# Kernel tuning notes

Measured on AMD Instinct MI355X. Metric: run time of the kernel, lower is better.

The kernel has to match this reference:

```python
import jax, jax.numpy as jnp
import numpy as np

N = 100000
E = 1600000
D = 128  # out_dim == head_dim (num_heads = 1)


def setup_inputs() -> dict:
    key = jax.random.key(0)
    ks = jax.random.split(key, 16)
    s = 0.05
    inp = {
        "h": jax.random.normal(ks[0], (N, D), dtype=jnp.float32),
        "c": jax.random.normal(ks[1], (N, 3), dtype=jnp.float32),
        "src": jax.random.randint(ks[2], (E,), 0, N),
        "dst": jax.random.randint(ks[3], (E,), 0, N),
        # Q/K/V projections (use_bias=False)
        "Wq": jax.random.normal(ks[4], (D, D), dtype=jnp.float32) * s,
        "Wk": jax.random.normal(ks[5], (D, D), dtype=jnp.float32) * s,
        "Wv": jax.random.normal(ks[6], (D, D), dtype=jnp.float32) * s,
        # linear_p: Linear(3,3) -> ReLU -> Linear(3,D)
        "Wp1": jax.random.normal(ks[7], (3, 3), dtype=jnp.float32) * s,
        "bp1": jnp.zeros((3,), dtype=jnp.float32),
        "Wp2": jax.random.normal(ks[8], (3, D), dtype=jnp.float32) * s,
        "bp2": jnp.zeros((D,), dtype=jnp.float32),
        # edge MLP: Linear(D,D) -> ReLU -> Linear(D,1)
        "We1": jax.random.normal(ks[9], (D, D), dtype=jnp.float32) * s,
        "be1": jnp.zeros((D,), dtype=jnp.float32),
        "We2": jax.random.normal(ks[10], (D, 1), dtype=jnp.float32) * s,
        "be2": jnp.zeros((1,), dtype=jnp.float32),
        # output projection O (has bias)
        "Wo": jax.random.normal(ks[11], (D, D), dtype=jnp.float32) * s,
        "bo": jnp.zeros((D,), dtype=jnp.float32),
    }
    return inp


def reference(h, c, src, dst, Wq, Wk, Wv, Wp1, bp1, Wp2, bp2,
              We1, be1, We2, be2, Wo, bo):
    scale = np.sqrt(np.float32(D))  # sqrt(out_dim) used by scaled_exp
    n = h.shape[0]
    # node projections
    Q = h @ Wq                                   # [N, D]
    K = h @ Wk                                   # [N, D]
    V = h @ Wv                                   # [N, D]
    P = jax.nn.relu(c @ Wp1 + bp1) @ Wp2 + bp2   # [N, D] position encoding
    # per-edge point-transformer score: MLP(K[src] - Q[dst] + P[src])
    dif = K[src] - Q[dst] + P[src]               # [E, D]
    raw = jax.nn.relu(dif @ We1 + be1) @ We2 + be2  # [E, 1]
    score = jnp.exp(jnp.clip(raw / scale, -5.0, 5.0))  # [E, 1]
    # gather-multiply-scatter: weighted V+P sum and normalizer z per dst node
    msg = (V + P)[src] * score                   # [E, D]
    wV = jax.ops.segment_sum(msg, dst, num_segments=n)    # [N, D]
    z = jax.ops.segment_sum(score, dst, num_segments=n)   # [N, 1]
    head_out = wV / z                            # [N, D]
    return head_out @ Wo + bo                    # [N, D]
```

## Files before the change

### kernel.cpp

```cpp
#include <hip/hip_runtime.h>
#include <math.h>

#define DD 128
#define CAP 10240
typedef unsigned int u32;
typedef unsigned short u16;
typedef __attribute__((ext_vector_type(8))) short bf16x8;
typedef __attribute__((ext_vector_type(4))) float f32x4;
typedef __attribute__((ext_vector_type(2))) float f32x2;

__device__ __forceinline__ float4 f4zero() { return make_float4(0.f, 0.f, 0.f, 0.f); }
__device__ __forceinline__ u32 bf16rne(float f) {
    u32 u = __float_as_uint(f);
    u += 0x7FFFu + ((u >> 16) & 1u);
    return u >> 16;
}
__device__ __forceinline__ u32 pack2(float lo, float hi) {
    return bf16rne(lo) | (bf16rne(hi) << 16);
}
__device__ __forceinline__ float unlo(u32 u) { return __uint_as_float(u << 16); }
__device__ __forceinline__ float unhi(u32 u) { return __uint_as_float(u & 0xFFFF0000u); }

__global__ __launch_bounds__(256) void fused_pre(
    const float* __restrict__ Wq, const float* __restrict__ Wk,
    const float* __restrict__ Wv, const float* __restrict__ We1,
    const float* __restrict__ be1, const float* __restrict__ Wp2,
    const float* __restrict__ bp2, const float* __restrict__ Wo,
    u32* __restrict__ BF,
    const int* __restrict__ src, const int* __restrict__ dst,
    int* __restrict__ gcount, u32* __restrict__ ebuf, int E) {
    const int t = threadIdx.x;
    if (blockIdx.x < 38) {
        const int bid = blockIdx.x * 4 + (t >> 6);
        const int l = t & 63;
        const int c = l & 15;
        const int kg = l >> 4;
        float val[8];

        if (bid < 120) {
            const int ct = bid / 5, ks = bid - ct * 5;
            const int u = ct / 6, r = ct - u * 6;
            const int n = 32 * u + 16 * (r < 2 ? r : (r & 1)) + c;
#pragma unroll
            for (int j = 0; j < 8; ++j) {
                const int k = ks * 32 + kg * 8 + j;
                float v = 0.f;
                if (r < 2) {
                    if (k < 128) {
                        float a = 0.f;
                        for (int q = 0; q < 128; ++q)
                            a = fmaf(Wq[k * 128 + q], We1[q * 128 + n], a);
                        v = a;
                    }
                } else if (r < 4) {
                    if (k < 128) {
                        float a = 0.f;
                        for (int q = 0; q < 128; ++q)
                            a = fmaf(Wk[k * 128 + q], We1[q * 128 + n], a);
                        v = a;
                    } else if (k < 131) {
                        float a = 0.f;
                        for (int q = 0; q < 128; ++q)
                            a = fmaf(Wp2[(k - 128) * 128 + q], We1[q * 128 + n], a);
                        v = a;
                    } else if (k == 131) {
                        float a = be1[n];
                        for (int q = 0; q < 128; ++q)
                            a = fmaf(bp2[q], We1[q * 128 + n], a);
                        v = a;
                    }
                } else {
                    if (k < 128) v = Wv[k * 128 + n];
                    else if (k < 131) v = Wp2[(k - 128) * 128 + n];
                    else if (k == 131) v = bp2[n];
                }
                val[j] = v;
            }
        } else {
            const int b2 = bid - 120;
            const int ct = b2 >> 2, ks = b2 & 3;
            const int n = ct * 16 + c;
#pragma unroll
            for (int j = 0; j < 8; ++j) {
                const int k = ks * 32 + kg * 8 + j;
                val[j] = Wo[k * 128 + n];
            }
        }
        u32* dp = &BF[((size_t)bid * 64 + l) * 4];
        dp[0] = pack2(val[0], val[1]);
        dp[1] = pack2(val[2], val[3]);
        dp[2] = pack2(val[4], val[5]);
        dp[3] = pack2(val[6], val[7]);
    } else {
        __shared__ int hist[256];
        __shared__ int base[256];
        hist[t] = 0;
        __syncthreads();
        const int chunk = (blockIdx.x - 38) * 4096;
        int bk[16], rk[16];
        u32 pv[16];
#pragma unroll
        for (int i = 0; i < 16; ++i) {
            int idx = chunk + i * 256 + t;
            bk[i] = -1;
            if (idx < E) {
                int dd = dst[idx];
                int ss = src[idx];
                bk[i] = dd >> 9;
                pv[i] = ((u32)ss << 9) | (u32)(dd & 511);
                rk[i] = atomicAdd(&hist[bk[i]], 1);
            }
        }
        __syncthreads();
        if (hist[t]) base[t] = t * CAP + atomicAdd(&gcount[t], hist[t]);
        __syncthreads();
#pragma unroll
        for (int i = 0; i < 16; ++i) {
            if (bk[i] >= 0) ebuf[base[bk[i]] + rk[i]] = pv[i];
        }
    }
}

__global__ __launch_bounds__(256) void scanB_we2r(
    const int* __restrict__ gcount, int* __restrict__ bucket_base,
    const float* __restrict__ We2, float* __restrict__ We2r) {
    __shared__ int s[256];
    int t = threadIdx.x;
    int orig = gcount[t];
    s[t] = orig;
    __syncthreads();
    for (int off = 1; off < 256; off <<= 1) {
        int x = (t >= off) ? s[t - off] : 0;
        __syncthreads();
        s[t] += x;
        __syncthreads();
    }
    bucket_base[t] = s[t] - orig;
    if (t < 128) {
        int col = 32 * (t >> 5) + 16 * (t & 1) + ((t & 31) >> 1);
        We2r[t] = We2[col];
    }
}

__global__ __launch_bounds__(256) void fused_mid(
    const float* __restrict__ h, const float* __restrict__ c,
    const float* __restrict__ Wp1, const float* __restrict__ bp1,
    const u32* __restrict__ BF,
    u32* __restrict__ QWb, u32* __restrict__ Vb,
    unsigned char* __restrict__ Kb8, int N,
    const int* __restrict__ gcount, const int* __restrict__ bucket_base,
    const u32* __restrict__ ebuf, int* __restrict__ ssrc,
    int* __restrict__ offs, int E, int NR) {
    __shared__ u32 lds[64 * 96];
    const int t = threadIdx.x;

    if ((int)blockIdx.x < NR) {
        int* cnt = (int*)lds;
        int* cur = cnt + 512;
        int* ts = cur + 512;
        const int r = blockIdx.x;
        const int cnt_r = gcount[r];
        const int base_r = bucket_base[r];
        cnt[t] = 0;
        cnt[t + 256] = 0;
        __syncthreads();
        const u32* eb = &ebuf[(size_t)r * CAP];
        for (int i = t; i < cnt_r; i += 256) atomicAdd(&cnt[eb[i] & 511], 1);
        __syncthreads();
        int v0 = cnt[2 * t], v1 = cnt[2 * t + 1];
        int pair = v0 + v1;
        ts[t] = pair;
        __syncthreads();
        for (int off = 1; off < 256; off <<= 1) {
            int x = (t >= off) ? ts[t - off] : 0;
            __syncthreads();
            ts[t] += x;
            __syncthreads();
        }
        int ex = ts[t] - pair;
        cur[2 * t] = ex;
        cur[2 * t + 1] = ex + v0;
        offs[r * 512 + 2 * t] = base_r + ex;
        offs[r * 512 + 2 * t + 1] = base_r + ex + v0;
        if (r == NR - 1 && t == 255) offs[NR * 512] = E;
        __syncthreads();
        for (int i = t; i < cnt_r; i += 256) {
            u32 e = eb[i];
            int p = atomicAdd(&cur[e & 511], 1);
            ssrc[base_r + p] = (int)(e >> 9);
        }
    } else {
        u32* hs = lds;
        const int row0 = ((int)blockIdx.x - NR) * 64;

#pragma unroll
        for (int i = 0; i < 8; ++i) {
            int f = t + i * 256;
            int row = f >> 5;
            int cq = f & 31;
            float4 v = f4zero();
            if (row0 + row < N) v = *(const float4*)&h[(size_t)(row0 + row) * DD + cq * 4];
            int idx = row * 96 + ((cq * 2) ^ ((row & 7) << 2));
            uint2 p;
            p.x = pack2(v.x, v.y);
            p.y = pack2(v.z, v.w);
            *(uint2*)&hs[idx] = p;
        }
        if (t < 64) {
            int row = t;
            float u0 = 0.f, u1 = 0.f, u2 = 0.f;
            if (row0 + row < N) {
                const float* cr = &c[(size_t)(row0 + row) * 3];
                float c0 = cr[0], c1 = cr[1], c2 = cr[2];
                u0 = fmaxf(bp1[0] + c0 * Wp1[0] + c1 * Wp1[3] + c2 * Wp1[6], 0.f);
                u1 = fmaxf(bp1[1] + c0 * Wp1[1] + c1 * Wp1[4] + c2 * Wp1[7], 0.f);
                u2 = fmaxf(bp1[2] + c0 * Wp1[2] + c1 * Wp1[5] + c2 * Wp1[8], 0.f);
            }
            int swz = (row & 7) << 2;
            uint4 z0 = make_uint4(pack2(u0, u1), pack2(u2, 1.0f), 0u, 0u);
            uint4 zz = make_uint4(0u, 0u, 0u, 0u);
#pragma unroll
            for (int q = 0; q < 4; ++q) {
                int idx = row * 96 + 64 + ((q * 4) ^ swz);
                *(uint4*)&hs[idx] = (q == 0) ? z0 : zz;
            }
        }
        __syncthreads();

        const int w = t >> 6, l = t & 63;
        const int cc = l & 15, kg = l >> 4;

        f32x4 acc[4][6];
#pragma unroll
        for (int rt = 0; rt < 4; ++rt)
#pragma unroll
            for (int r = 0; r < 6; ++r) acc[rt][r] = (f32x4){0.f, 0.f, 0.f, 0.f};

#pragma unroll
        for (int ks = 0; ks < 5; ++ks) {
            bf16x8 a[4];
#pragma unroll
            for (int rt = 0; rt < 4; ++rt) {
                int row = rt * 16 + cc;
                int idx = row * 96 + ((ks * 16 + kg * 4) ^ ((row & 7) << 2));
                a[rt] = *(const bf16x8*)&hs[idx];
            }
#pragma unroll
            for (int r = 0; r < 6; ++r) {
                const bf16x8 b = *(const bf16x8*)&BF[(((size_t)(w * 6 + r) * 5 + ks) * 64 + l) * 4];
#pragma unroll
                for (int rt = 0; rt < 4; ++rt)
                    acc[rt][r] = __builtin_amdgcn_mfma_f32_16x16x32_bf16(a[rt], b, acc[rt][r], 0, 0, 0);
            }
        }

#pragma unroll
        for (int rt = 0; rt < 4; ++rt) {
#pragma unroll
            for (int j = 0; j < 4; ++j) {
                int row = row0 + rt * 16 + kg * 4 + j;
                if (row >= N) continue;
                QWb[(size_t)row * 64 + w * 16 + cc] = pack2(acc[rt][0][j], acc[rt][1][j]);
                Vb[(size_t)row * 64 + w * 16 + cc] = pack2(acc[rt][4][j], acc[rt][5][j]);
                u32 kp = __builtin_amdgcn_cvt_pk_fp8_f32(acc[rt][2][j], acc[rt][3][j], 0u, false);
                *(u16*)&Kb8[(size_t)row * 128 + w * 32 + cc * 2] = (u16)kp;
            }
        }
    }
}

__global__ __launch_bounds__(256) void aggregate(
    const int* __restrict__ offs, const int* __restrict__ ssrc,
    const unsigned char* __restrict__ Kb8, const u32* __restrict__ Vb,
    const u32* __restrict__ QWb, const float* __restrict__ We2r,
    const float* __restrict__ be2, u32* __restrict__ headb, int N) {
    const int node = (blockIdx.x * 256 + threadIdx.x) >> 6;
    const int lane = threadIdx.x & 63;
    if (node >= N) return;
    const int g = lane >> 4, i = lane & 15;

    const float INVS = 0.08838834764831845f;

    uint4 Qu = *(const uint4*)&QWb[(size_t)node * 64 + 4 * i];
    float q0 = unlo(Qu.x), q1 = unhi(Qu.x), q2 = unlo(Qu.y), q3 = unhi(Qu.y);
    float q4 = unlo(Qu.z), q5 = unhi(Qu.z), q6 = unlo(Qu.w), q7 = unhi(Qu.w);
    float4 wA = *(const float4*)&We2r[8 * i];
    float4 wB = *(const float4*)&We2r[8 * i + 4];
    float b2 = be2[0];

    const int beg = offs[node], end = offs[node + 1];
    float a0 = 0.f, a1 = 0.f, a2 = 0.f, a3 = 0.f;
    float a4 = 0.f, a5 = 0.f, a6 = 0.f, a7 = 0.f;
    float zacc = 0.f;

    int e = beg + g;
    int s = (e < end) ? ssrc[e] : 0;
    for (int e0 = beg; e0 < end; e0 += 4) {
        const bool act = (e0 + g) < end;
        const int scur = s;
        const int en = e0 + 4 + g;
        s = (en < end) ? ssrc[en] : 0;

        uint2 kk = *(const uint2*)&Kb8[(size_t)scur * 128 + 8 * i];
        uint4 va = *(const uint4*)&Vb[(size_t)scur * 64 + 4 * i];

        f32x2 f0 = __builtin_amdgcn_cvt_pk_f32_fp8(kk.x, false);
        f32x2 f1 = __builtin_amdgcn_cvt_pk_f32_fp8(kk.x, true);
        f32x2 f2 = __builtin_amdgcn_cvt_pk_f32_fp8(kk.y, false);
        f32x2 f3 = __builtin_amdgcn_cvt_pk_f32_fp8(kk.y, true);

        float p;
        p = fmaxf(f0[0] - q0, 0.f) * wA.x;
        p = fmaf(fmaxf(f0[1] - q1, 0.f), wA.y, p);
        p = fmaf(fmaxf(f1[0] - q2, 0.f), wA.z, p);
        p = fmaf(fmaxf(f1[1] - q3, 0.f), wA.w, p);
        p = fmaf(fmaxf(f2[0] - q4, 0.f), wB.x, p);
        p = fmaf(fmaxf(f2[1] - q5, 0.f), wB.y, p);
        p = fmaf(fmaxf(f3[0] - q6, 0.f), wB.z, p);
        p = fmaf(fmaxf(f3[1] - q7, 0.f), wB.w, p);
#pragma unroll
        for (int off = 1; off <= 8; off <<= 1) p += __shfl_xor(p, off);

        float sc = act ? __expf(fminf(fmaxf((p + b2) * INVS, -5.f), 5.f)) : 0.f;

        a0 = fmaf(unlo(va.x), sc, a0);
        a1 = fmaf(unhi(va.x), sc, a1);
        a2 = fmaf(unlo(va.y), sc, a2);
        a3 = fmaf(unhi(va.y), sc, a3);
        a4 = fmaf(unlo(va.z), sc, a4);
        a5 = fmaf(unhi(va.z), sc, a5);
        a6 = fmaf(unlo(va.w), sc, a6);
        a7 = fmaf(unhi(va.w), sc, a7);
        zacc += sc;
    }

    a0 += __shfl_xor(a0, 16); a0 += __shfl_xor(a0, 32);
    a1 += __shfl_xor(a1, 16); a1 += __shfl_xor(a1, 32);
    a2 += __shfl_xor(a2, 16); a2 += __shfl_xor(a2, 32);
    a3 += __shfl_xor(a3, 16); a3 += __shfl_xor(a3, 32);
    a4 += __shfl_xor(a4, 16); a4 += __shfl_xor(a4, 32);
    a5 += __shfl_xor(a5, 16); a5 += __shfl_xor(a5, 32);
    a6 += __shfl_xor(a6, 16); a6 += __shfl_xor(a6, 32);
    a7 += __shfl_xor(a7, 16); a7 += __shfl_xor(a7, 32);
    zacc += __shfl_xor(zacc, 16); zacc += __shfl_xor(zacc, 32);

    if (g == 0) {
        float rz = 1.0f / zacc;
        uint4 o;
        o.x = pack2(a0 * rz, a1 * rz);
        o.y = pack2(a2 * rz, a3 * rz);
        o.z = pack2(a4 * rz, a5 * rz);
        o.w = pack2(a6 * rz, a7 * rz);
        *(uint4*)&headb[(size_t)node * 64 + 4 * i] = o;
    }
}

__global__ __launch_bounds__(256) void out_mfma(
    const u32* __restrict__ headb, const u32* __restrict__ WoF,
    const float* __restrict__ bo, float* __restrict__ out, int N) {
    __shared__ u32 hs[64 * 64];

    const int row0 = blockIdx.x * 64;
    const int t = threadIdx.x;

#pragma unroll
    for (int i = 0; i < 4; ++i) {
        int f = t + i * 256;
        int row = f >> 4;
        int cq = f & 15;
        uint4 v = make_uint4(0u, 0u, 0u, 0u);
        if (row0 + row < N) v = *(const uint4*)&headb[(size_t)(row0 + row) * 64 + cq * 4];
        int m = cq >> 2;
        int cb = (cq & 3) * 4;
        int swz = (row & 7) << 2;
        uint2 A, B;
        A.x = (v.x & 0xFFFFu) | (v.y << 16);
        A.y = (v.z & 0xFFFFu) | (v.w << 16);
        B.x = (v.x >> 16) | (v.y & 0xFFFF0000u);
        B.y = (v.z >> 16) | (v.w & 0xFFFF0000u);
        int dA = 16 * m + (cb >> 1);
        *(uint2*)&hs[row * 64 + (dA ^ swz)] = A;
        *(uint2*)&hs[row * 64 + ((dA + 8) ^ swz)] = B;
    }
    __syncthreads();

    const int w = t >> 6, l = t & 63;
    const int cc = l & 15, kg = l >> 4;

    f32x4 acc[4][2];
#pragma unroll
    for (int rt = 0; rt < 4; ++rt) {
        acc[rt][0] = (f32x4){0.f, 0.f, 0.f, 0.f};
        acc[rt][1] = (f32x4){0.f, 0.f, 0.f, 0.f};
    }

#pragma unroll
    for (int ks = 0; ks < 4; ++ks) {
        bf16x8 a[4];
#pragma unroll
        for (int rt = 0; rt < 4; ++rt) {
            int row = rt * 16 + cc;
            int idx = row * 64 + ((ks * 16 + kg * 4) ^ ((row & 7) << 2));
            a[rt] = *(const bf16x8*)&hs[idx];
        }
#pragma unroll
        for (int ctl = 0; ctl < 2; ++ctl) {
            const bf16x8 b = *(const bf16x8*)&WoF[(((size_t)(2 * w + ctl) * 4 + ks) * 64 + l) * 4];
#pragma unroll
            for (int rt = 0; rt < 4; ++rt)
                acc[rt][ctl] = __builtin_amdgcn_mfma_f32_16x16x32_bf16(a[rt], b, acc[rt][ctl], 0, 0, 0);
        }
    }

#pragma unroll
    for (int ctl = 0; ctl < 2; ++ctl) {
        int col = (2 * w + ctl) * 16 + cc;
        float bias = bo[col];
#pragma unroll
        for (int rt = 0; rt < 4; ++rt) {
#pragma unroll
            for (int j = 0; j < 4; ++j) {
                int row = row0 + rt * 16 + kg * 4 + j;
                if (row >= N) continue;
                out[(size_t)row * DD + col] = acc[rt][ctl][j] + bias;
            }
        }
    }
}

extern "C" void kernel_launch(void* const* d_in, const int* in_sizes, int n_in,
                              void* d_out, int out_size, void* d_ws, size_t ws_size,
                              hipStream_t stream) {
    const float* h   = (const float*)d_in[0];
    const float* c   = (const float*)d_in[1];
    const int*   src = (const int*)d_in[2];
    const int*   dst = (const int*)d_in[3];
    const float* Wq  = (const float*)d_in[4];
    const float* Wk  = (const float*)d_in[5];
    const float* Wv  = (const float*)d_in[6];
    const float* Wp1 = (const float*)d_in[7];
    const float* bp1 = (const float*)d_in[8];
    const float* Wp2 = (const float*)d_in[9];
    const float* bp2 = (const float*)d_in[10];
    const float* We1 = (const float*)d_in[11];
    const float* be1 = (const float*)d_in[12];
    const float* We2 = (const float*)d_in[13];
    const float* be2 = (const float*)d_in[14];
    const float* Wo  = (const float*)d_in[15];
    const float* bo  = (const float*)d_in[16];

    const int N = in_sizes[0] / DD;
    const int E = in_sizes[2];
    const int NR = (N + 511) >> 9;

    u32* BF    = (u32*)d_ws;
    u32* WoF   = BF + 120 * 256;
    u32* QWb   = BF + 152 * 256;
    u32* Vb    = QWb + (size_t)N * 64;
    unsigned char* Kb8 = (unsigned char*)(Vb + (size_t)N * 64);
    u32* headb = (u32*)(Kb8 + (size_t)N * 128);
    int* offs  = (int*)(headb + (size_t)N * 64);
    int* gcount = offs + ((size_t)NR * 512 + 1);
    int* bbase  = gcount + 256;
    float* We2r = (float*)(bbase + 256);
    int* ssrc   = (int*)(We2r + 128);
    u32* ebuf   = (u32*)(ssrc + E);

    const int NB1 = (E + 4095) / 4096;

    hipMemsetAsync(gcount, 0, 256 * sizeof(int), stream);

    fused_pre<<<38 + NB1, 256, 0, stream>>>(Wq, Wk, Wv, We1, be1, Wp2, bp2, Wo,
                                            BF, src, dst, gcount, ebuf, E);

    scanB_we2r<<<1, 256, 0, stream>>>(gcount, bbase, We2, We2r);

    fused_mid<<<NR + (N + 63) / 64, 256, 0, stream>>>(
        h, c, Wp1, bp1, BF, QWb, Vb, Kb8, N,
        gcount, bbase, ebuf, ssrc, offs, E, NR);

    aggregate<<<(N * 64 + 255) / 256, 256, 0, stream>>>(offs, ssrc, Kb8, Vb,
                                                        QWb, We2r, be2, headb, N);

    out_mfma<<<(N + 63) / 64, 256, 0, stream>>>(headb, WoF, bo, (float*)d_out, N);
}
```

Baseline: 210.1 us.

## Regroup pipeline kernels and widen per-lane work in edge aggregation

Splits weight-fragment composition into its own small kernel and fuses the edge bucketing pass with the node projection GEMM. The local per-bucket sort moves into a separate kernel after the scan. The aggregate kernel now has each lane handle 16 features with 8 edges in flight per node, using exp2 with a prescaled constant. Workspace layout is reordered. This changes kernel overlap and memory-level parallelism in the gather, at the cost of an extra launch and higher register pressure.

After: 236.5 us. 1.13x slower.

```diff
diff --git a/kernel.cpp b/kernel.cpp
--- a/kernel.cpp
+++ b/kernel.cpp
@@ -21,82 +21,92 @@
 __device__ __forceinline__ float unlo(u32 u) { return __uint_as_float(u << 16); }
 __device__ __forceinline__ float unhi(u32 u) { return __uint_as_float(u & 0xFFFF0000u); }
 
-__global__ __launch_bounds__(256) void fused_pre(
+__global__ __launch_bounds__(256) void compose_frags(
     const float* __restrict__ Wq, const float* __restrict__ Wk,
     const float* __restrict__ Wv, const float* __restrict__ We1,
     const float* __restrict__ be1, const float* __restrict__ Wp2,
     const float* __restrict__ bp2, const float* __restrict__ Wo,
-    u32* __restrict__ BF,
+    u32* __restrict__ BF) {
+    const int t = threadIdx.x;
+    const int bid = blockIdx.x * 4 + (t >> 6);
+    const int l = t & 63;
+    const int c = l & 15;
+    const int kg = l >> 4;
+    float val[8];
+
+    if (bid < 120) {
+        const int ct = bid / 5, ks = bid - ct * 5;
+        const int u = ct / 6, r = ct - u * 6;
+        const int n = 32 * u + 16 * (r < 2 ? r : (r & 1)) + c;
+#pragma unroll
+        for (int j = 0; j < 8; ++j) {
+            const int k = ks * 32 + kg * 8 + j;
+            float v = 0.f;
+            if (r < 2) {
+                if (k < 128) {
+                    float a = 0.f;
+                    for (int q = 0; q < 128; ++q)
+                        a = fmaf(Wq[k * 128 + q], We1[q * 128 + n], a);
+                    v = a;
+                }
+            } else if (r < 4) {
+                if (k < 128) {
+                    float a = 0.f;
+                    for (int q = 0; q < 128; ++q)
+                        a = fmaf(Wk[k * 128 + q], We1[q * 128 + n], a);
+                    v = a;
+                } else if (k < 131) {
+                    float a = 0.f;
+                    for (int q = 0; q < 128; ++q)
+                        a = fmaf(Wp2[(k - 128) * 128 + q], We1[q * 128 + n], a);
+                    v = a;
+                } else if (k == 131) {
+                    float a = be1[n];
+                    for (int q = 0; q < 128; ++q)
+                        a = fmaf(bp2[q], We1[q * 128 + n], a);
+                    v = a;
+                }
+            } else {
+                if (k < 128) v = Wv[k * 128 + n];
+                else if (k < 131) v = Wp2[(k - 128) * 128 + n];
+                else if (k == 131) v = bp2[n];
+            }
+            val[j] = v;
+        }
+    } else {
+        const int b2 = bid - 120;
+        const int ct = b2 >> 2, ks = b2 & 3;
+        const int n = ct * 16 + c;
+#pragma unroll
+        for (int j = 0; j < 8; ++j) {
+            const int k = ks * 32 + kg * 8 + j;
+            val[j] = Wo[k * 128 + n];
+        }
+    }
+    u32* dp = &BF[((size_t)bid * 64 + l) * 4];
+    dp[0] = pack2(val[0], val[1]);
+    dp[1] = pack2(val[2], val[3]);
+    dp[2] = pack2(val[4], val[5]);
+    dp[3] = pack2(val[6], val[7]);
+}
+
+__global__ __launch_bounds__(256) void fused_p1_gemm(
+    const float* __restrict__ h, const float* __restrict__ c,
+    const float* __restrict__ Wp1, const float* __restrict__ bp1,
+    const u32* __restrict__ BF,
+    u32* __restrict__ QWb, unsigned char* __restrict__ Kb8,
+    u32* __restrict__ Vb, int N,
     const int* __restrict__ src, const int* __restrict__ dst,
-    int* __restrict__ gcount, u32* __restrict__ ebuf, int E) {
+    int* __restrict__ gcount, u32* __restrict__ ebuf, int E, int NB1) {
+    __shared__ u32 lds[64 * 96];
     const int t = threadIdx.x;
-    if (blockIdx.x < 38) {
-        const int bid = blockIdx.x * 4 + (t >> 6);
-        const int l = t & 63;
-        const int c = l & 15;
-        const int kg = l >> 4;
-        float val[8];
-
-        if (bid < 120) {
-            const int ct = bid / 5, ks = bid - ct * 5;
-            const int u = ct / 6, r = ct - u * 6;
-            const int n = 32 * u + 16 * (r < 2 ? r : (r & 1)) + c;
-#pragma unroll
-            for (int j = 0; j < 8; ++j) {
-                const int k = ks * 32 + kg * 8 + j;
-                float v = 0.f;
-                if (r < 2) {
-                    if (k < 128) {
-                        float a = 0.f;
-                        for (int q = 0; q < 128; ++q)
-                            a = fmaf(Wq[k * 128 + q], We1[q * 128 + n], a);
-                        v = a;
-                    }
-                } else if (r < 4) {
-                    if (k < 128) {
-                        float a = 0.f;
-                        for (int q = 0; q < 128; ++q)
-                            a = fmaf(Wk[k * 128 + q], We1[q * 128 + n], a);
-                        v = a;
-                    } else if (k < 131) {
-                        float a = 0.f;
-                        for (int q = 0; q < 128; ++q)
-                            a = fmaf(Wp2[(k - 128) * 128 + q], We1[q * 128 + n], a);
-                        v = a;
-                    } else if (k == 131) {
-                        float a = be1[n];
-                        for (int q = 0; q < 128; ++q)
-                            a = fmaf(bp2[q], We1[q * 128 + n], a);
-                        v = a;
-                    }
-                } else {
-                    if (k < 128) v = Wv[k * 128 + n];
-                    else if (k < 131) v = Wp2[(k - 128) * 128 + n];
-                    else if (k == 131) v = bp2[n];
-                }
-                val[j] = v;
-            }
-        } else {
-            const int b2 = bid - 120;
-            const int ct = b2 >> 2, ks = b2 & 3;
-            const int n = ct * 16 + c;
-#pragma unroll
-            for (int j = 0; j < 8; ++j) {
-                const int k = ks * 32 + kg * 8 + j;
-                val[j] = Wo[k * 128 + n];
-            }
-        }
-        u32* dp = &BF[((size_t)bid * 64 + l) * 4];
-        dp[0] = pack2(val[0], val[1]);
-        dp[1] = pack2(val[2], val[3]);
-        dp[2] = pack2(val[4], val[5]);
-        dp[3] = pack2(val[6], val[7]);
-    } else {
-        __shared__ int hist[256];
-        __shared__ int base[256];
+
+    if ((int)blockIdx.x < NB1) {
+        int* hist = (int*)lds;
+        int* base = hist + 256;
         hist[t] = 0;
         __syncthreads();
-        const int chunk = (blockIdx.x - 38) * 4096;
+        const int chunk = blockIdx.x * 4096;
         int bk[16], rk[16];
         u32 pv[16];
 #pragma unroll
@@ -118,80 +128,9 @@
         for (int i = 0; i < 16; ++i) {
             if (bk[i] >= 0) ebuf[base[bk[i]] + rk[i]] = pv[i];
         }
-    }
-}
-
-__global__ __launch_bounds__(256) void scanB_we2r(
-    const int* __restrict__ gcount, int* __restrict__ bucket_base,
-    const float* __restrict__ We2, float* __restrict__ We2r) {
-    __shared__ int s[256];
-    int t = threadIdx.x;
-    int orig = gcount[t];
-    s[t] = orig;
-    __syncthreads();
-    for (int off = 1; off < 256; off <<= 1) {
-        int x = (t >= off) ? s[t - off] : 0;
-        __syncthreads();
-        s[t] += x;
-        __syncthreads();
-    }
-    bucket_base[t] = s[t] - orig;
-    if (t < 128) {
-        int col = 32 * (t >> 5) + 16 * (t & 1) + ((t & 31) >> 1);
-        We2r[t] = We2[col];
-    }
-}
-
-__global__ __launch_bounds__(256) void fused_mid(
-    const float* __restrict__ h, const float* __restrict__ c,
-    const float* __restrict__ Wp1, const float* __restrict__ bp1,
-    const u32* __restrict__ BF,
-    u32* __restrict__ QWb, u32* __restrict__ Vb,
-    unsigned char* __restrict__ Kb8, int N,
-    const int* __restrict__ gcount, const int* __restrict__ bucket_base,
-    const u32* __restrict__ ebuf, int* __restrict__ ssrc,
-    int* __restrict__ offs, int E, int NR) {
-    __shared__ u32 lds[64 * 96];
-    const int t = threadIdx.x;
-
-    if ((int)blockIdx.x < NR) {
-        int* cnt = (int*)lds;
-        int* cur = cnt + 512;
-        int* ts = cur + 512;
-        const int r = blockIdx.x;
-        const int cnt_r = gcount[r];
-        const int base_r = bucket_base[r];
-        cnt[t] = 0;
-        cnt[t + 256] = 0;
-        __syncthreads();
-        const u32* eb = &ebuf[(size_t)r * CAP];
-        for (int i = t; i < cnt_r; i += 256) atomicAdd(&cnt[eb[i] & 511], 1);
-        __syncthreads();
-        int v0 = cnt[2 * t], v1 = cnt[2 * t + 1];
-        int pair = v0 + v1;
-        ts[t] = pair;
-        __syncthreads();
-        for (int off = 1; off < 256; off <<= 1) {
-            int x = (t >= off) ? ts[t - off] : 0;
-            __syncthreads();
-            ts[t] += x;
-            __syncthreads();
-        }
-        int ex = ts[t] - pair;
-        cur[2 * t] = ex;
-        cur[2 * t + 1] = ex + v0;
-        offs[r * 512 + 2 * t] = base_r + ex;
-        offs[r * 512 + 2 * t + 1] = base_r + ex + v0;
-        if (r == NR - 1 && t == 255) offs[NR * 512] = E;
-        __syncthreads();
-        for (int i = t; i < cnt_r; i += 256) {
-            u32 e = eb[i];
-            int p = atomicAdd(&cur[e & 511], 1);
-            ssrc[base_r + p] = (int)(e >> 9);
-        }
     } else {
         u32* hs = lds;
-        const int row0 = ((int)blockIdx.x - NR) * 64;
+        const int row0 = ((int)blockIdx.x - NB1) * 64;
 
 #pragma unroll
         for (int i = 0; i < 8; ++i) {
@@ -261,11 +200,73 @@
                 int row = row0 + rt * 16 + kg * 4 + j;
                 if (row >= N) continue;
                 QWb[(size_t)row * 64 + w * 16 + cc] = pack2(acc[rt][0][j], acc[rt][1][j]);
-                Vb[(size_t)row * 64 + w * 16 + cc] = pack2(acc[rt][4][j], acc[rt][5][j]);
                 u32 kp = __builtin_amdgcn_cvt_pk_fp8_f32(acc[rt][2][j], acc[rt][3][j], 0u, false);
                 *(u16*)&Kb8[(size_t)row * 128 + w * 32 + cc * 2] = (u16)kp;
-            }
-        }
+                Vb[(size_t)row * 64 + w * 16 + cc] = pack2(acc[rt][4][j], acc[rt][5][j]);
+            }
+        }
+    }
+}
+
+__global__ __launch_bounds__(256) void scanB_we2r(
+    const int* __restrict__ gcount, int* __restrict__ bucket_base,
+    const float* __restrict__ We2, float* __restrict__ We2r) {
+    __shared__ int s[256];
+    int t = threadIdx.x;
+    int orig = gcount[t];
+    s[t] = orig;
+    __syncthreads();
+    for (int off = 1; off < 256; off <<= 1) {
+        int x = (t >= off) ? s[t - off] : 0;
+        __syncthreads();
+        s[t] += x;
+        __syncthreads();
+    }
+    bucket_base[t] = s[t] - orig;
+    if (t < 128) {
+        int col = 32 * (t >> 5) + 16 * (t & 1) + ((t & 31) >> 1);
+        We2r[t] = We2[col];
+    }
+}
+
+__global__ __launch_bounds__(256) void p2_local(
+    const int* __restrict__ gcount, const int* __restrict__ bucket_base,
+    const u32* __restrict__ ebuf, int* __restrict__ ssrc,
+    int* __restrict__ offs, int E, int NR) {
+    __shared__ int cnt[512];
+    __shared__ int cur[512];
+    __shared__ int ts[256];
+    const int r = blockIdx.x;
+    const int t = threadIdx.x;
+    const int cnt_r = gcount[r];
+    const int base_r = bucket_base[r];
+    cnt[t] = 0;
+    cnt[t + 256] = 0;
+    __syncthreads();
+    const u32* eb = &ebuf[(size_t)r * CAP];
+    for (int i = t; i < cnt_r; i += 256) atomicAdd(&cnt[eb[i] & 511], 1);
+    __syncthreads();
+    int v0 = cnt[2 * t], v1 = cnt[2 * t + 1];
+    int pair = v0 + v1;
+    ts[t] = pair;
+    __syncthreads();
+    for (int off = 1; off < 256; off <<= 1) {
+        int x = (t >= off) ? ts[t - off] : 0;
+        __syncthreads();
+        ts[t] += x;
+        __syncthreads();
+    }
+    int ex = ts[t] - pair;
+    cur[2 * t] = ex;
+    cur[2 * t + 1] = ex + v0;
+    offs[r * 512 + 2 * t] = base_r + ex;
+    offs[r * 512 + 2 * t + 1] = base_r + ex + v0;
+    if (r == NR - 1 && t == 255) offs[NR * 512] = E;
+    __syncthreads();
+    for (int i = t; i < cnt_r; i += 256) {
+        u32 e = eb[i];
+        int p = atomicAdd(&cur[e & 511], 1);
+        ssrc[base_r + p] = (int)(e >> 9);
     }
 }
 
@@ -277,81 +278,105 @@
     const int node = (blockIdx.x * 256 + threadIdx.x) >> 6;
     const int lane = threadIdx.x & 63;
     if (node >= N) return;
-    const int g = lane >> 4, i = lane & 15;
-
-    const float INVS = 0.08838834764831845f;
-
-    uint4 Qu = *(const uint4*)&QWb[(size_t)node * 64 + 4 * i];
-    float q0 = unlo(Qu.x), q1 = unhi(Qu.x), q2 = unlo(Qu.y), q3 = unhi(Qu.y);
-    float q4 = unlo(Qu.z), q5 = unhi(Qu.z), q6 = unlo(Qu.w), q7 = unhi(Qu.w);
-    float4 wA = *(const float4*)&We2r[8 * i];
-    float4 wB = *(const float4*)&We2r[8 * i + 4];
+    const int g = lane >> 3, i = lane & 7;
+
+    const float SC = 0.08838834764831845f * 1.4426950408889634f;
+    const float CL = 5.0f * 1.4426950408889634f;
+
+    uint4 QA = *(const uint4*)&QWb[(size_t)node * 64 + 8 * i];
+    uint4 QB = *(const uint4*)&QWb[(size_t)node * 64 + 8 * i + 4];
+    float q[16];
+    q[0] = unlo(QA.x); q[1] = unhi(QA.x); q[2] = unlo(QA.y); q[3] = unhi(QA.y);
+    q[4] = unlo(QA.z); q[5] = unhi(QA.z); q[6] = unlo(QA.w); q[7] = unhi(QA.w);
+    q[8] = unlo(QB.x); q[9] = unhi(QB.x); q[10] = unlo(QB.y); q[11] = unhi(QB.y);
+    q[12] = unlo(QB.z); q[13] = unhi(QB.z); q[14] = unlo(QB.w); q[15] = unhi(QB.w);
+
+    float4 w0 = *(const float4*)&We2r[16 * i];
+    float4 w1 = *(const float4*)&We2r[16 * i + 4];
+    float4 w2 = *(const float4*)&We2r[16 * i + 8];
+    float4 w3 = *(const float4*)&We2r[16 * i + 12];
+    float w[16] = {w0.x, w0.y, w0.z, w0.w, w1.x, w1.y, w1.z, w1.w,
+                   w2.x, w2.y, w2.z, w2.w, w3.x, w3.y, w3.z, w3.w};
     float b2 = be2[0];
 
     const int beg = offs[node], end = offs[node + 1];
-    float a0 = 0.f, a1 = 0.f, a2 = 0.f, a3 = 0.f;
-    float a4 = 0.f, a5 = 0.f, a6 = 0.f, a7 = 0.f;
+    float acc[16];
+#pragma unroll
+    for (int j = 0; j < 16; ++j) acc[j] = 0.f;
     float zacc = 0.f;
 
     int e = beg + g;
     int s = (e < end) ? ssrc[e] : 0;
-    for (int e0 = beg; e0 < end; e0 += 4) {
+    for (int e0 = beg; e0 < end; e0 += 8) {
         const bool act = (e0 + g) < end;
         const int scur = s;
-        const int en = e0 + 4 + g;
+        const int en = e0 + 8 + g;
         s = (en < end) ? ssrc[en] : 0;
 
-        uint2 kk = *(const uint2*)&Kb8[(size_t)scur * 128 + 8 * i];
-        uint4 va = *(const uint4*)&Vb[(size_t)scur * 64 + 4 * i];
-
-        f32x2 f0 = __builtin_amdgcn_cvt_pk_f32_fp8(kk.x, false);
-        f32x2 f1 = __builtin_amdgcn_cvt_pk_f32_fp8(kk.x, true);
-        f32x2 f2 = __builtin_amdgcn_cvt_pk_f32_fp8(kk.y, false);
-        f32x2 f3 = __builtin_amdgcn_cvt_pk_f32_fp8(kk.y, true);
-
-        float p;
-        p = fmaxf(f0[0] - q0, 0.f) * wA.x;
-        p = fmaf(fmaxf(f0[1] - q1, 0.f), wA.y, p);
-        p = fmaf(fmaxf(f1[0] - q2, 0.f), wA.z, p);
-        p = fmaf(fmaxf(f1[1] - q3, 0.f), wA.w, p);
-        p = fmaf(fmaxf(f2[0] - q4, 0.f), wB.x, p);
-        p = fmaf(fmaxf(f2[1] - q5, 0.f), wB.y, p);
-        p = fmaf(fmaxf(f3[0] - q6, 0.f), wB.z, p);
-        p = fmaf(fmaxf(f3[1] - q7, 0.f), wB.w, p);
-#pragma unroll
-        for (int off = 1; off <= 8; off <<= 1) p += __shfl_xor(p, off);
-
-        float sc = act ? __expf(fminf(fmaxf((p + b2) * INVS, -5.f), 5.f)) : 0.f;
-
-        a0 = fmaf(unlo(va.x), sc, a0);
-        a1 = fmaf(unhi(va.x), sc, a1);
-        a2 = fmaf(unlo(va.y), sc, a2);
-        a3 = fmaf(unhi(va.y), sc, a3);
-        a4 = fmaf(unlo(va.z), sc, a4);
-        a5 = fmaf(unhi(va.z), sc, a5);
-        a6 = fmaf(unlo(va.w), sc, a6);
-        a7 = fmaf(unhi(va.w), sc, a7);
+        uint4 kk = *(const uint4*)&Kb8[(size_t)scur * 128 + 16 * i];
+        uint4 va = *(const uint4*)&Vb[(size_t)scur * 64 + 8 * i];
+        uint4 vb = *(const uint4*)&Vb[(size_t)scur * 64 + 8 * i + 4];
+
+        float kd[16];
+        f32x2 tt;
+        tt = __builtin_amdgcn_cvt_pk_f32_fp8(kk.x, false); kd[0] = tt[0]; kd[1] = tt[1];
+        tt = __builtin_amdgcn_cvt_pk_f32_fp8(kk.x, true);  kd[2] = tt[0]; kd[3] = tt[1];
+        tt = __builtin_amdgcn_cvt_pk_f32_fp8(kk.y, false); kd[4] = tt[0]; kd[5] = tt[1];
+        tt = __builtin_amdgcn_cvt_pk_f32_fp8(kk.y, true);  kd[6] = tt[0]; kd[7] = tt[1];
+        tt = __builtin_amdgcn_cvt_pk_f32_fp8(kk.z, false); kd[8] = tt[0]; kd[9] = tt[1];
+        tt = __builtin_amdgcn_cvt_pk_f32_fp8(kk.z, true);  kd[10] = tt[0]; kd[11] = tt[1];
+        tt = __builtin_amdgcn_cvt_pk_f32_fp8(kk.w, false); kd[12] = tt[0]; kd[13] = tt[1];
+        tt = __builtin_amdgcn_cvt_pk_f32_fp8(kk.w, true);  kd[14] = tt[0]; kd[15] = tt[1];
+
+        float p = fmaxf(kd[0] - q[0], 0.f) * w[0];
+#pragma unroll
+        for (int j = 1; j < 16; ++j) p = fmaf(fmaxf(kd[j] - q[j], 0.f), w[j], p);
+#pragma unroll
+        for (int off = 1; off <= 4; off <<= 1) p += __shfl_xor(p, off);
+
+        float targ = (p + b2) * SC;
+        targ = fminf(fmaxf(targ, -CL), CL);
+        float sc = act ? exp2f(targ) : 0.f;
+
+        acc[0]  = fmaf(unlo(va.x), sc, acc[0]);
+        acc[1]  = fmaf(unhi(va.x), sc, acc[1]);
+        acc[2]  = fmaf(unlo(va.y), sc, acc[2]);
+        acc[3]  = fmaf(unhi(va.y), sc, acc[3]);
+        acc[4]  = fmaf(unlo(va.z), sc, acc[4]);
+        acc[5]  = fmaf(unhi(va.z), sc, acc[5]);
+        acc[6]  = fmaf(unlo(va.w), sc, acc[6]);
+        acc[7]  = fmaf(unhi(va.w), sc, acc[7]);
+        acc[8]  = fmaf(unlo(vb.x), sc, acc[8]);
+        acc[9]  = fmaf(unhi(vb.x), sc, acc[9]);
+        acc[10] = fmaf(unlo(vb.y), sc, acc[10]);
+        acc[11] = fmaf(unhi(vb.y), sc, acc[11]);
+        acc[12] = fmaf(unlo(vb.z), sc, acc[12]);
+        acc[13] = fmaf(unhi(vb.z), sc, acc[13]);
+        acc[14] = fmaf(unlo(vb.w), sc, acc[14]);
+        acc[15] = fmaf(unhi(vb.w), sc, acc[15]);
         zacc += sc;
     }
 
-    a0 += __shfl_xor(a0, 16); a0 += __shfl_xor(a0, 32);
-    a1 += __shfl_xor(a1, 16); a1 += __shfl_xor(a1, 32);
-    a2 += __shfl_xor(a2, 16); a2 += __shfl_xor(a2, 32);
-    a3 += __shfl_xor(a3, 16); a3 += __shfl_xor(a3, 32);
-    a4 += __shfl_xor(a4, 16); a4 += __shfl_xor(a4, 32);
-    a5 += __shfl_xor(a5, 16); a5 += __shfl_xor(a5, 32);
-    a6 += __shfl_xor(a6, 16); a6 += __shfl_xor(a6, 32);
-    a7 += __shfl_xor(a7, 16); a7 += __shfl_xor(a7, 32);
-    zacc += __shfl_xor(zacc, 16); zacc += __shfl_xor(zacc, 32);
+#pragma unroll
+    for (int off = 8; off <= 32; off <<= 1) {
+#pragma unroll
+        for (int j = 0; j < 16; ++j) acc[j] += __shfl_xor(acc[j], off);
+        zacc += __shfl_xor(zacc, off);
+    }
 
     if (g == 0) {
         float rz = 1.0f / zacc;
-        uint4 o;
-        o.x = pack2(a0 * rz, a1 * rz);
-        o.y = pack2(a2 * rz, a3 * rz);
-        o.z = pack2(a4 * rz, a5 * rz);
-        o.w = pack2(a6 * rz, a7 * rz);
-        *(uint4*)&headb[(size_t)node * 64 + 4 * i] = o;
+        uint4 oA, oB;
+        oA.x = pack2(acc[0] * rz, acc[1] * rz);
+        oA.y = pack2(acc[2] * rz, acc[3] * rz);
+        oA.z = pack2(acc[4] * rz, acc[5] * rz);
+        oA.w = pack2(acc[6] * rz, acc[7] * rz);
+        oB.x = pack2(acc[8] * rz, acc[9] * rz);
+        oB.y = pack2(acc[10] * rz, acc[11] * rz);
+        oB.z = pack2(acc[12] * rz, acc[13] * rz);
+        oB.w = pack2(acc[14] * rz, acc[15] * rz);
+        *(uint4*)&headb[(size_t)node * 64 + 8 * i] = oA;
+        *(uint4*)&headb[(size_t)node * 64 + 8 * i + 4] = oB;
     }
 }
 
@@ -452,13 +477,15 @@
     const int N = in_sizes[0] / DD;
     const int E = in_sizes[2];
     const int NR = (N + 511) >> 9;
+    const int NB1 = (E + 4095) / 4096;
+    const int NG = (N + 63) / 64;
 
     u32* BF    = (u32*)d_ws;
     u32* WoF   = BF + 120 * 256;
     u32* QWb   = BF + 152 * 256;
-    u32* Vb    = QWb + (size_t)N * 64;
-    unsigned char* Kb8 = (unsigned char*)(Vb + (size_t)N * 64);
-    u32* headb = (u32*)(Kb8 + (size_t)N * 128);
+    unsigned char* Kb8 = (unsigned char*)(QWb + (size_t)N * 64);
+    u32* Vb    = (u32*)(Kb8 + (size_t)N * 128);
+    u32* headb = Vb + (size_t)N * 64;
     int* offs  = (int*)(headb + (size_t)N * 64);
     int* gcount = offs + ((size_t)NR * 512 + 1);
     int* bbase  = gcount + 256;
@@ -466,21 +493,20 @@
     int* ssrc   = (int*)(We2r + 128);
     u32* ebuf   = (u32*)(ssrc + E);
 
-    const int NB1 = (E + 4095) / 4096;
-
     hipMemsetAsync(gcount, 0, 256 * sizeof(int), stream);
 
-    fused_pre<<<38 + NB1, 256, 0, stream>>>(Wq, Wk, Wv, We1, be1, Wp2, bp2, Wo,
-                                            BF, src, dst, gcount, ebuf, E);
+    compose_frags<<<38, 256, 0, stream>>>(Wq, Wk, Wv, We1, be1, Wp2, bp2, Wo, BF);
+
+    fused_p1_gemm<<<NB1 + NG, 256, 0, stream>>>(
+        h, c, Wp1, bp1, BF, QWb, Kb8, Vb, N,
+        src, dst, gcount, ebuf, E, NB1);
 
     scanB_we2r<<<1, 256, 0, stream>>>(gcount, bbase, We2, We2r);
 
-    fused_mid<<<NR + (N + 63) / 64, 256, 0, stream>>>(
-        h, c, Wp1, bp1, BF, QWb, Vb, Kb8, N,
-        gcount, bbase, ebuf, ssrc, offs, E, NR);
+    p2_local<<<NR, 256, 0, stream>>>(gcount, bbase, ebuf, ssrc, offs, E, NR);
 
     aggregate<<<(N * 64 + 255) / 256, 256, 0, stream>>>(offs, ssrc, Kb8, Vb,
                                                         QWb, We2r, be2, headb, N);
 
-    out_mfma<<<(N + 63) / 64, 256, 0, stream>>>(headb, WoF, bo, (float*)d_out, N);
-}
+    out_mfma<<<NG, 256, 0, stream>>>(headb, WoF, bo, (float*)d_out, N);
+}
```
